# Kernel tuning notes

Hardware: AMD Instinct MI355X
Metric: run time of the kernel (lower is better)

## Reference

```python
import jax, jax.numpy as jnp
import numpy as np

EPS = 1e-08


def _cdist(x):
    # x: [B, N, D] -> [B, N, N] Euclidean distances, safe-sqrt for grad at 0
    diff = x[:, :, None, :] - x[:, None, :, :]          # [B, N, N, D]
    sq = jnp.sum(diff * diff, axis=-1)                   # [B, N, N]
    pos = sq > 0
    return jnp.where(pos, jnp.sqrt(jnp.where(pos, sq, 1.0)), 0.0)


def setup_inputs() -> dict:
    key = jax.random.key(0)
    k1, k2, k3 = jax.random.split(key, 3)
    B, N, D = 32, 1024, 3
    preds = jax.random.normal(k1, (B, N, D), dtype=jnp.float32)
    targets = jax.random.normal(k2, (B, N, D), dtype=jnp.float32)
    mask = jax.random.randint(k3, (B, N), 0, 2, dtype=jnp.int32)
    return {"preds": preds, "targets": targets, "mask": mask}


def reference(preds, targets, mask):
    m = mask.astype(preds.dtype)                         # [B, N]
    diag_att = m[:, :, None] * m[:, None, :]            # [B, N, N]
    dist_preds = _cdist(preds)                           # [B, N, N]
    dist_targets = _cdist(targets)                       # [B, N, N]
    dist = jnp.abs(dist_preds - dist_targets) / (dist_targets + EPS)  # relative=True
    loss = dist * diag_att
    return loss.sum() / diag_att.sum()
```

## Files before the change

kernel.cpp:

```cpp
#include <hip/hip_runtime.h>


constexpr int NT    = 256;
constexpr int C     = 8;
constexpr int TRI   = C * (C + 1) / 2;
constexpr int CHMAX = 128;

__global__ __launch_bounds__(NT) void idl_tri(
    const float* __restrict__ preds, const float* __restrict__ targets,
    const int* __restrict__ mask, float* __restrict__ partials,
    float* __restrict__ counts)
{
    const int bid = blockIdx.x;
    const int b   = bid / TRI;
    int ca = 0, cb;
    {
        int s = bid % TRI, rem = C;
        while (s >= rem) { s -= rem; --rem; ++ca; }
        cb = ca + s;
    }
    const int tid  = threadIdx.x;
    const int wid  = tid >> 6, lane = tid & 63;
    const int N    = 1024;

    __shared__ __align__(16) float rpxs[CHMAX], rpys[CHMAX], rpzs[CHMAX];
    __shared__ __align__(16) float rtxs[CHMAX], rtys[CHMAX], rtzs[CHMAX];
    __shared__ __align__(16) float cpxs[CHMAX], cpys[CHMAX], cpzs[CHMAX];
    __shared__ __align__(16) float ctxs[CHMAX], ctys[CHMAX], ctzs[CHMAX];
    __shared__ int   s_wt[4][4];
    __shared__ float s_red[4];

    const float* pb = preds   + (size_t)b * N * 3;
    const float* tb = targets + (size_t)b * N * 3;
    const int*   mb = mask    + (size_t)b * N;

    int msk[4];
#pragma unroll
    for (int s = 0; s < 4; ++s) msk[s] = mb[s * NT + tid];
    unsigned long long bal[4];
#pragma unroll
    for (int s = 0; s < 4; ++s) bal[s] = __ballot(msk[s] != 0);
    if (lane == 0) {
#pragma unroll
        for (int s = 0; s < 4; ++s) s_wt[s][wid] = (int)__popcll(bal[s]);
    }
    __syncthreads();

    int base[4], run = 0;
#pragma unroll
    for (int s = 0; s < 4; ++s) {
#pragma unroll
        for (int w = 0; w < 4; ++w) {
            if (w == wid) base[s] = run;
            run += s_wt[s][w];
        }
    }
    const int K = run;

    const int ch  = 4 * ((K + 4 * C - 1) / (4 * C));
    const int ra0 = min(ca * ch, K), ra1 = min(ra0 + ch, K);
    const int cb0 = min(cb * ch, K), cb1 = min(cb0 + ch, K);
    const int rsz = ra1 - ra0;
    const int csz = cb1 - cb0;

    const unsigned long long lt = (1ull << lane) - 1ull;
#pragma unroll
    for (int s = 0; s < 4; ++s) {
        if (msk[s]) {
            const int  pos = base[s] + (int)__popcll(bal[s] & lt);
            const bool inR = (pos >= ra0) && (pos < ra1);
            const bool inC = (pos >= cb0) && (pos < cb1);
            if (inR | inC) {
                const int idx = s * NT + tid;
                const float ppx = pb[idx * 3 + 0], ppy = pb[idx * 3 + 1], ppz = pb[idx * 3 + 2];
                const float ttx = tb[idx * 3 + 0], tty = tb[idx * 3 + 1], ttz = tb[idx * 3 + 2];
                if (inR) {
                    const int r = pos - ra0;
                    rpxs[r] = ppx; rpys[r] = ppy; rpzs[r] = ppz;
                    rtxs[r] = ttx; rtys[r] = tty; rtzs[r] = ttz;
                }
                if (inC) {
                    const int c = pos - cb0;
                    cpxs[c] = ppx; cpys[c] = ppy; cpzs[c] = ppz;
                    ctxs[c] = ttx; ctys[c] = tty; ctzs[c] = ttz;
                }
            }
        }
    }
    __syncthreads();

    const int rq  = 4 * ((rsz + 15) / 16);
    const int lr0 = min(wid * rq, rsz);
    const int lr1 = min(lr0 + rq, rsz);

    float acc = 0.0f;
    for (int cp = 0; cp * 64 < csz; ++cp) {
        const int  jr = cp * 64 + lane;
        const bool jv = jr < csz;
        const int  j  = jv ? jr : 0;
        const float jpx = cpxs[j], jpy = cpys[j], jpz = cpzs[j];
        const float jtx = ctxs[j], jty = ctys[j], jtz = ctzs[j];

        for (int rg = lr0; rg < lr1; rg += 4) {
            const float4 r4x = *(const float4*)&rpxs[rg];
            const float4 r4y = *(const float4*)&rpys[rg];
            const float4 r4z = *(const float4*)&rpzs[rg];
            const float4 s4x = *(const float4*)&rtxs[rg];
            const float4 s4y = *(const float4*)&rtys[rg];
            const float4 s4z = *(const float4*)&rtzs[rg];
            const float rxa[4] = {r4x.x, r4x.y, r4x.z, r4x.w};
            const float rya[4] = {r4y.x, r4y.y, r4y.z, r4y.w};
            const float rza[4] = {r4z.x, r4z.y, r4z.z, r4z.w};
            const float sxa[4] = {s4x.x, s4x.y, s4x.z, s4x.w};
            const float sya[4] = {s4y.x, s4y.y, s4y.z, s4y.w};
            const float sza[4] = {s4z.x, s4z.y, s4z.z, s4z.w};
            const int nk = lr1 - rg;
#pragma unroll
            for (int k = 0; k < 4; ++k) {
                if (k < nk) {
                    const float dx = jpx - rxa[k], dy = jpy - rya[k], dz = jpz - rza[k];
                    const float sp = fmaf(dx, dx, fmaf(dy, dy, dz * dz));
                    const float dp = __builtin_amdgcn_sqrtf(sp);
                    const float ex = jtx - sxa[k], ey = jty - sya[k], ez = jtz - sza[k];
                    const float st = fmaf(ex, ex, fmaf(ey, ey, ez * ez));
                    const float rr = __builtin_amdgcn_rsqf(st);
                    const float dt = st * rr;
                    const float t  = fabsf(dp - dt) * rr;
                    acc += (jv && st > 0.0f) ? t : 0.0f;
                }
            }
        }
    }

    for (int off = 32; off > 0; off >>= 1) acc += __shfl_down(acc, off, 64);
    if (lane == 0) s_red[wid] = acc;
    __syncthreads();
    if (tid == 0) {
        float ssum = s_red[0] + s_red[1] + s_red[2] + s_red[3];
        if (ca != cb) ssum *= 2.0f;
        partials[bid] = ssum;
        if (ca == 0 && cb == 0) counts[b] = (float)K;
    }
}

__global__ __launch_bounds__(NT) void idl_final(
    const float* __restrict__ partials, int nP,
    const float* __restrict__ counts, int B, float* __restrict__ out)
{
    __shared__ float s_n[NT / 64], s_d[NT / 64];
    const int tid = threadIdx.x;
    float num = 0.0f, den = 0.0f;
    for (int i = tid; i < nP; i += NT) num += partials[i];
    for (int i = tid; i < B;  i += NT) { const float c = counts[i]; den = fmaf(c, c, den); }
    for (int off = 32; off > 0; off >>= 1) {
        num += __shfl_down(num, off, 64);
        den += __shfl_down(den, off, 64);
    }
    if ((tid & 63) == 0) { s_n[tid >> 6] = num; s_d[tid >> 6] = den; }
    __syncthreads();
    if (tid == 0) {
        float n = 0.0f, d = 0.0f;
#pragma unroll
        for (int w = 0; w < NT / 64; ++w) { n += s_n[w]; d += s_d[w]; }
        out[0] = n / d;
    }
}

extern "C" void kernel_launch(void* const* d_in, const int* in_sizes, int n_in,
                              void* d_out, int out_size, void* d_ws, size_t ws_size,
                              hipStream_t stream)
{
    const float* preds   = (const float*)d_in[0];
    const float* targets = (const float*)d_in[1];
    const int*   mask    = (const int*)d_in[2];
    const int N = 1024;
    const int B = in_sizes[2] / N;

    float* ws       = (float*)d_ws;
    const int nBlocks = B * TRI;
    float* partials = ws;
    float* counts   = ws + nBlocks;

    idl_tri  <<<dim3(nBlocks), NT, 0, stream>>>(preds, targets, mask, partials, counts);
    idl_final<<<dim3(1),       NT, 0, stream>>>(partials, nBlocks, counts, B, (float*)d_out);
}
```

Baseline: 16.86 us.

## Precompute compacted SoA point arrays in a separate kernel before pair tiles

Adds a per-batch compaction kernel that scans the mask once and writes the masked points into a structure-of-arrays buffer in workspace. The pair-tile blocks then load their row and column chunks from that buffer with float4 loads, so they no longer each re-read the full mask, redo the ballot prefix scan and gather strided AoS coordinates. This removes redundant work repeated across the 36 blocks per batch, but adds a third kernel launch and a round trip through global memory.

```diff
diff --git a/kernel.cpp b/kernel.cpp
--- a/kernel.cpp
+++ b/kernel.cpp
@@ -5,11 +5,67 @@
 constexpr int C     = 8;
 constexpr int TRI   = C * (C + 1) / 2;
 constexpr int CHMAX = 128;
+constexpr int NPTS  = 1024;
+
+
+__global__ __launch_bounds__(NT) void idl_compact(
+    const float* __restrict__ preds, const float* __restrict__ targets,
+    const int* __restrict__ mask, float* __restrict__ ws, int B, int soaOff)
+{
+    const int b = blockIdx.x, tid = threadIdx.x;
+    const int wid = tid >> 6, lane = tid & 63;
+    __shared__ int s_wt[4][4];
+
+    const int*   mb = mask    + (size_t)b * NPTS;
+    const float* pb = preds   + (size_t)b * NPTS * 3;
+    const float* tb = targets + (size_t)b * NPTS * 3;
+    float*       db = ws + soaOff + (size_t)b * 6 * NPTS;
+
+    int msk[4];
+#pragma unroll
+    for (int s = 0; s < 4; ++s) msk[s] = mb[s * NT + tid];
+    unsigned long long bal[4];
+#pragma unroll
+    for (int s = 0; s < 4; ++s) bal[s] = __ballot(msk[s] != 0);
+    if (lane == 0) {
+#pragma unroll
+        for (int s = 0; s < 4; ++s) s_wt[s][wid] = (int)__popcll(bal[s]);
+    }
+    __syncthreads();
+
+    int base[4], run = 0;
+#pragma unroll
+    for (int s = 0; s < 4; ++s) {
+#pragma unroll
+        for (int w = 0; w < 4; ++w) {
+            if (w == wid) base[s] = run;
+            run += s_wt[s][w];
+        }
+    }
+    const int K = run;
+
+    const unsigned long long lt = (1ull << lane) - 1ull;
+#pragma unroll
+    for (int s = 0; s < 4; ++s) {
+        if (msk[s]) {
+            const int idx = s * NT + tid;
+            const int pos = base[s] + (int)__popcll(bal[s] & lt);
+            db[0 * NPTS + pos] = pb[idx * 3 + 0];
+            db[1 * NPTS + pos] = pb[idx * 3 + 1];
+            db[2 * NPTS + pos] = pb[idx * 3 + 2];
+            db[3 * NPTS + pos] = tb[idx * 3 + 0];
+            db[4 * NPTS + pos] = tb[idx * 3 + 1];
+            db[5 * NPTS + pos] = tb[idx * 3 + 2];
+        }
+    }
+    if (tid == 0) {
+        ws[b] = (float)K;
+        ((int*)ws)[B + b] = K;
+    }
+}
 
 __global__ __launch_bounds__(NT) void idl_tri(
-    const float* __restrict__ preds, const float* __restrict__ targets,
-    const int* __restrict__ mask, float* __restrict__ partials,
-    float* __restrict__ counts)
+    const float* __restrict__ ws, float* __restrict__ partials, int B, int soaOff)
 {
     const int bid = blockIdx.x;
     const int b   = bid / TRI;
@@ -19,43 +75,15 @@
         while (s >= rem) { s -= rem; --rem; ++ca; }
         cb = ca + s;
     }
-    const int tid  = threadIdx.x;
-    const int wid  = tid >> 6, lane = tid & 63;
-    const int N    = 1024;
-
-    __shared__ __align__(16) float rpxs[CHMAX], rpys[CHMAX], rpzs[CHMAX];
-    __shared__ __align__(16) float rtxs[CHMAX], rtys[CHMAX], rtzs[CHMAX];
-    __shared__ __align__(16) float cpxs[CHMAX], cpys[CHMAX], cpzs[CHMAX];
-    __shared__ __align__(16) float ctxs[CHMAX], ctys[CHMAX], ctzs[CHMAX];
-    __shared__ int   s_wt[4][4];
+    const int tid = threadIdx.x;
+    const int wid = tid >> 6, lane = tid & 63;
+
+    __shared__ __align__(16) float Rw[6][CHMAX];
+    __shared__ __align__(16) float Cw[6][CHMAX];
     __shared__ float s_red[4];
 
-    const float* pb = preds   + (size_t)b * N * 3;
-    const float* tb = targets + (size_t)b * N * 3;
-    const int*   mb = mask    + (size_t)b * N;
-
-    int msk[4];
-#pragma unroll
-    for (int s = 0; s < 4; ++s) msk[s] = mb[s * NT + tid];
-    unsigned long long bal[4];
-#pragma unroll
-    for (int s = 0; s < 4; ++s) bal[s] = __ballot(msk[s] != 0);
-    if (lane == 0) {
-#pragma unroll
-        for (int s = 0; s < 4; ++s) s_wt[s][wid] = (int)__popcll(bal[s]);
-    }
-    __syncthreads();
-
-    int base[4], run = 0;
-#pragma unroll
-    for (int s = 0; s < 4; ++s) {
-#pragma unroll
-        for (int w = 0; w < 4; ++w) {
-            if (w == wid) base[s] = run;
-            run += s_wt[s][w];
-        }
-    }
-    const int K = run;
+    const int    K  = ((const int*)ws)[B + b];
+    const float* db = ws + soaOff + (size_t)b * 6 * NPTS;
 
     const int ch  = 4 * ((K + 4 * C - 1) / (4 * C));
     const int ra0 = min(ca * ch, K), ra1 = min(ra0 + ch, K);
@@ -63,28 +91,15 @@
     const int rsz = ra1 - ra0;
     const int csz = cb1 - cb0;
 
-    const unsigned long long lt = (1ull << lane) - 1ull;
-#pragma unroll
-    for (int s = 0; s < 4; ++s) {
-        if (msk[s]) {
-            const int  pos = base[s] + (int)__popcll(bal[s] & lt);
-            const bool inR = (pos >= ra0) && (pos < ra1);
-            const bool inC = (pos >= cb0) && (pos < cb1);
-            if (inR | inC) {
-                const int idx = s * NT + tid;
-                const float ppx = pb[idx * 3 + 0], ppy = pb[idx * 3 + 1], ppz = pb[idx * 3 + 2];
-                const float ttx = tb[idx * 3 + 0], tty = tb[idx * 3 + 1], ttz = tb[idx * 3 + 2];
-                if (inR) {
-                    const int r = pos - ra0;
-                    rpxs[r] = ppx; rpys[r] = ppy; rpzs[r] = ppz;
-                    rtxs[r] = ttx; rtys[r] = tty; rtzs[r] = ttz;
-                }
-                if (inC) {
-                    const int c = pos - cb0;
-                    cpxs[c] = ppx; cpys[c] = ppy; cpzs[c] = ppz;
-                    ctxs[c] = ttx; ctys[c] = tty; ctzs[c] = ttz;
-                }
-            }
+    {
+        const int u = tid;
+        if (u < 6 * (CHMAX / 4)) {
+            const int a = u >> 5;
+            const int g = u & 31;
+            if (4 * g < rsz)
+                *(float4*)&Rw[a][4 * g] = *(const float4*)&db[a * NPTS + ra0 + 4 * g];
+            if (4 * g < csz)
+                *(float4*)&Cw[a][4 * g] = *(const float4*)&db[a * NPTS + cb0 + 4 * g];
         }
     }
     __syncthreads();
@@ -98,16 +113,16 @@
         const int  jr = cp * 64 + lane;
         const bool jv = jr < csz;
         const int  j  = jv ? jr : 0;
-        const float jpx = cpxs[j], jpy = cpys[j], jpz = cpzs[j];
-        const float jtx = ctxs[j], jty = ctys[j], jtz = ctzs[j];
+        const float jpx = Cw[0][j], jpy = Cw[1][j], jpz = Cw[2][j];
+        const float jtx = Cw[3][j], jty = Cw[4][j], jtz = Cw[5][j];
 
         for (int rg = lr0; rg < lr1; rg += 4) {
-            const float4 r4x = *(const float4*)&rpxs[rg];
-            const float4 r4y = *(const float4*)&rpys[rg];
-            const float4 r4z = *(const float4*)&rpzs[rg];
-            const float4 s4x = *(const float4*)&rtxs[rg];
-            const float4 s4y = *(const float4*)&rtys[rg];
-            const float4 s4z = *(const float4*)&rtzs[rg];
+            const float4 r4x = *(const float4*)&Rw[0][rg];
+            const float4 r4y = *(const float4*)&Rw[1][rg];
+            const float4 r4z = *(const float4*)&Rw[2][rg];
+            const float4 s4x = *(const float4*)&Rw[3][rg];
+            const float4 s4y = *(const float4*)&Rw[4][rg];
+            const float4 s4z = *(const float4*)&Rw[5][rg];
             const float rxa[4] = {r4x.x, r4x.y, r4x.z, r4x.w};
             const float rya[4] = {r4y.x, r4y.y, r4y.z, r4y.w};
             const float rza[4] = {r4z.x, r4z.y, r4z.z, r4z.w};
@@ -139,7 +154,6 @@
         float ssum = s_red[0] + s_red[1] + s_red[2] + s_red[3];
         if (ca != cb) ssum *= 2.0f;
         partials[bid] = ssum;
-        if (ca == 0 && cb == 0) counts[b] = (float)K;
     }
 }
 
@@ -176,11 +190,12 @@
     const int N = 1024;
     const int B = in_sizes[2] / N;
 
-    float* ws       = (float*)d_ws;
+    float* ws = (float*)d_ws;
     const int nBlocks = B * TRI;
-    float* partials = ws;
-    float* counts   = ws + nBlocks;
-
-    idl_tri  <<<dim3(nBlocks), NT, 0, stream>>>(preds, targets, mask, partials, counts);
-    idl_final<<<dim3(1),       NT, 0, stream>>>(partials, nBlocks, counts, B, (float*)d_out);
-}
+    const int soaOff  = 2 * B + nBlocks + ((2 * B + nBlocks) % 4 ? 4 - (2 * B + nBlocks) % 4 : 0);
+    float* partials = ws + 2 * B;
+
+    idl_compact<<<dim3(B),       NT, 0, stream>>>(preds, targets, mask, ws, B, soaOff);
+    idl_tri    <<<dim3(nBlocks), NT, 0, stream>>>(ws, partials, B, soaOff);
+    idl_final  <<<dim3(1),       NT, 0, stream>>>(partials, nBlocks, ws, B, (float*)d_out);
+}
```

Result: slower. 20.96 us (+24.3%).
